# Kernel optimization log

Measured on AMD Instinct MI355X. Metric: run time of the kernel, lower is better.

Reference implementation:

```python
import jax, jax.numpy as jnp
import numpy as np

N_VAR, N_CONS = 100_000, 50_000
N_FEAS = N_VAR + N_CONS
E_OBJ, E_FEAS = 1_600_000, 2_400_000
H_OBJ = H_CONS = 64
C = H_OBJ + H_CONS  # concat_dim = 128
D = 256             # decoder_hidden_channels
NUM_GRAPHS = 64


def _gcn(x, src, dst, ew, W, b):
    # PyG GCNConv with edge weights: add self-loops (weight 1), sym-normalize, aggregate at dst.
    n = x.shape[0]
    loop = jnp.arange(n)
    src_f = jnp.concatenate([src, loop])
    dst_f = jnp.concatenate([dst, loop])
    ew_f = jnp.concatenate([ew, jnp.ones((n,), ew.dtype)])
    deg = jax.ops.segment_sum(ew_f, dst_f, num_segments=n)
    dinv = jnp.where(deg > 0, jax.lax.rsqrt(deg), 0.0)
    coef = dinv[src_f] * ew_f * dinv[dst_f]            # [E+n]
    h = x @ W                                          # [n, H]
    out = jax.ops.segment_sum(coef[:, None] * h[src_f], dst_f, num_segments=n)
    return out + b


def _mlp(z, W1, b1, W2, b2):
    return jnp.maximum(z @ W1 + b1, 0.0) @ W2 + b2


def setup_inputs() -> dict:
    key = jax.random.key(0)
    ks = iter(jax.random.split(key, 64))

    def nrm(shape, scale=1.0):
        return jax.random.normal(next(ks), shape, jnp.float32) * scale

    def lin(i, o):
        return nrm((i, o), 1.0 / np.sqrt(i)), jnp.zeros((o,), jnp.float32)

    inp = {}
    inp['x_obj'] = nrm((N_VAR, 4))
    inp['ei_obj'] = jax.random.randint(next(ks), (2, E_OBJ), 0, N_VAR)
    inp['ew_obj'] = jax.random.uniform(next(ks), (E_OBJ,), jnp.float32)
    inp['x_feas'] = nrm((N_FEAS, 4))
    inp['ei_feas'] = jax.random.randint(next(ks), (2, E_FEAS), 0, N_FEAS)
    inp['ew_feas'] = jax.random.uniform(next(ks), (E_FEAS,), jnp.float32)
    inp['batch_var'] = jnp.sort(jax.random.randint(next(ks), (N_VAR,), 0, NUM_GRAPHS))
    inp['n_var'] = N_VAR
    inp['n_bin'] = 50_000
    inp['c1o_W'], inp['c1o_b'] = lin(4, H_OBJ)
    inp['c2o_W'], inp['c2o_b'] = lin(H_OBJ, H_OBJ)
    inp['c1c_W'], inp['c1c_b'] = lin(4, H_CONS)
    inp['c2c_W'], inp['c2c_b'] = lin(H_CONS, H_CONS)
    inp['mu_W'], inp['mu_b'] = lin(C, C)
    inp['lv_W'], inp['lv_b'] = lin(C, C)
    inp['dx_W1'], inp['dx_b1'] = lin(C, D)
    inp['dx_W2'], inp['dx_b2'] = lin(D, 1)
    inp['dc_W1'], inp['dc_b1'] = lin(C, D)
    inp['dc_W2'], inp['dc_b2'] = lin(D, 1)
    inp['dk_W1'], inp['dk_b1'] = lin(C, D)
    inp['dk_W2'], inp['dk_b2'] = lin(D, 1)
    inp['di_W1'], inp['di_b1'] = lin(C, D)
    inp['di_W2'], inp['di_b2'] = lin(D, 1)
    return inp


def reference(x_obj, ei_obj, ew_obj, x_feas, ei_feas, ew_feas, batch_var, n_var, n_bin,
              c1o_W, c1o_b, c2o_W, c2o_b, c1c_W, c1c_b, c2c_W, c2c_b,
              mu_W, mu_b, lv_W, lv_b,
              dx_W1, dx_b1, dx_W2, dx_b2, dc_W1, dc_b1, dc_W2, dc_b2,
              dk_W1, dk_b1, dk_W2, dk_b2, di_W1, di_b1, di_W2, di_b2):
    so, do = ei_obj[0], ei_obj[1]
    sf, df = ei_feas[0], ei_feas[1]
    # objective encoder (all nodes are variables)
    h = jax.nn.relu(_gcn(x_obj, so, do, ew_obj, c1o_W, c1o_b))
    z_obj_var = jax.nn.relu(_gcn(h, so, do, ew_obj, c2o_W, c2o_b))
    # constraints encoder
    h = jax.nn.relu(_gcn(x_feas, sf, df, ew_feas, c1c_W, c1c_b))
    h = jax.nn.relu(_gcn(h, sf, df, ew_feas, c2c_W, c2c_b))
    z_cons_var = h[:n_var]          # variable_mask == first n_var nodes
    z_cons_constraints = h[n_var:]
    z_var = jnp.concatenate([z_obj_var, z_cons_var], axis=1)        # [N_var, C]
    z_cons_pad = jnp.pad(z_cons_constraints, ((0, 0), (0, C - z_cons_constraints.shape[1])))
    z_shared = jnp.concatenate([z_var, z_cons_pad], axis=0)         # [N_feas, C]
    z_mu = z_shared @ mu_W + mu_b
    z_logvar = z_shared @ lv_W + lv_b
    eps = jax.random.normal(jax.random.key(1), z_mu.shape, z_mu.dtype)
    z = z_mu + jnp.exp(0.5 * z_logvar) * eps
    z_var_s = z[:n_var]
    z_con_s = z[n_var:]
    x_hat = _mlp(z_var_s, dx_W1, dx_b1, dx_W2, dx_b2)[:, 0]
    # global_mean_pool over variable nodes
    sums = jax.ops.segment_sum(z_var_s, batch_var, num_segments=NUM_GRAPHS)
    cnts = jax.ops.segment_sum(jnp.ones((z_var_s.shape[0],), z.dtype), batch_var, num_segments=NUM_GRAPHS)
    pooled = sums / jnp.maximum(cnts, 1.0)[:, None]
    predicted_cost = _mlp(pooled, dc_W1, dc_b1, dc_W2, dc_b2)[:, 0]
    predicted_constraints = _mlp(z_con_s, dk_W1, dk_b1, dk_W2, dk_b2)[:, 0]
    integrality = jax.nn.sigmoid(_mlp(z_var_s, di_W1, di_b1, di_W2, di_b2))[:, 0]
    predicted_integrality = integrality[:n_bin]  # binary_mask == first n_bin variables
    return (x_hat, predicted_cost, predicted_constraints, predicted_integrality, z_mu, z_logvar)
```

## Files before the change

### kernel.cpp

```cpp
#include <hip/hip_runtime.h>
#include <math.h>

#define N_VAR_C  100000
#define N_CONS_C 50000
#define N_FEAS_C 150000
#define E_OBJ_C  1600000
#define E_FEAS_C 2400000
#define NG 64
#define N_BIN_C 50000
#define CAP 48

#define X_HAT_OFF 0
#define COST_OFF  100000
#define CONS_OFF  100064
#define INTG_OFF  150064
#define ZMU_OFF   200064
#define ZEL_TOTAL (N_FEAS_C * 128)
#define ZLV_OFF   (ZMU_OFF + ZEL_TOTAL)

static __device__ __forceinline__ unsigned rotl32(unsigned x, unsigned r) {
  return (x << r) | (x >> (32u - r));
}

static __device__ __forceinline__ void threefry01(unsigned x0, unsigned x1,
                                                  unsigned& o0, unsigned& o1) {
  const unsigned ks0 = 0u, ks1 = 1u, ks2 = 0x1BD11BDAu ^ 0u ^ 1u;
  x0 += ks0; x1 += ks1;
  x0 += x1; x1 = rotl32(x1, 13); x1 ^= x0;
  x0 += x1; x1 = rotl32(x1, 15); x1 ^= x0;
  x0 += x1; x1 = rotl32(x1, 26); x1 ^= x0;
  x0 += x1; x1 = rotl32(x1, 6);  x1 ^= x0;
  x0 += ks1; x1 += ks2 + 1u;
  x0 += x1; x1 = rotl32(x1, 17); x1 ^= x0;
  x0 += x1; x1 = rotl32(x1, 29); x1 ^= x0;
  x0 += x1; x1 = rotl32(x1, 16); x1 ^= x0;
  x0 += x1; x1 = rotl32(x1, 24); x1 ^= x0;
  x0 += ks2; x1 += ks0 + 2u;
  x0 += x1; x1 = rotl32(x1, 13); x1 ^= x0;
  x0 += x1; x1 = rotl32(x1, 15); x1 ^= x0;
  x0 += x1; x1 = rotl32(x1, 26); x1 ^= x0;
  x0 += x1; x1 = rotl32(x1, 6);  x1 ^= x0;
  x0 += ks0; x1 += ks1 + 3u;
  x0 += x1; x1 = rotl32(x1, 17); x1 ^= x0;
  x0 += x1; x1 = rotl32(x1, 29); x1 ^= x0;
  x0 += x1; x1 = rotl32(x1, 16); x1 ^= x0;
  x0 += x1; x1 = rotl32(x1, 24); x1 ^= x0;
  x0 += ks1; x1 += ks2 + 4u;
  x0 += x1; x1 = rotl32(x1, 13); x1 ^= x0;
  x0 += x1; x1 = rotl32(x1, 15); x1 ^= x0;
  x0 += x1; x1 = rotl32(x1, 26); x1 ^= x0;
  x0 += x1; x1 = rotl32(x1, 6);  x1 ^= x0;
  x0 += ks2; x1 += ks0 + 5u;
  o0 = x0; o1 = x1;
}

static __device__ __forceinline__ float bits_to_normal(unsigned b) {
  float f = __uint_as_float(0x3F800000u | (b >> 9)) - 1.0f;
  const float lo = -0.99999994f;
  float u = f * 2.0f + lo;
  u = fmaxf(lo, u);
  float w = -log1pf(-u * u);
  float p;
  if (w < 5.0f) {
    w -= 2.5f;
    p = 2.81022636e-08f;
    p = fmaf(p, w, 3.43273939e-07f);
    p = fmaf(p, w, -3.5233877e-06f);
    p = fmaf(p, w, -4.39150654e-06f);
    p = fmaf(p, w, 0.00021858087f);
    p = fmaf(p, w, -0.00125372503f);
    p = fmaf(p, w, -0.00417768164f);
    p = fmaf(p, w, 0.246640727f);
    p = fmaf(p, w, 1.50140941f);
  } else {
    w = sqrtf(w) - 3.0f;
    p = -0.000200214257f;
    p = fmaf(p, w, 0.000100950558f);
    p = fmaf(p, w, 0.00134934322f);
    p = fmaf(p, w, -0.00367342844f);
    p = fmaf(p, w, 0.00573950773f);
    p = fmaf(p, w, -0.0076224613f);
    p = fmaf(p, w, 0.00943887047f);
    p = fmaf(p, w, 1.00167406f);
    p = fmaf(p, w, 2.83297682f);
  }
  return 1.41421354f * (p * u);
}

__global__ __launch_bounds__(256) void fill_slots_kernel(
    const int* __restrict__ src, const int* __restrict__ dst,
    const float* __restrict__ ew, int* __restrict__ cnt,
    int2* __restrict__ slots, int E) {
  int e = blockIdx.x * 256 + threadIdx.x;
  if (e >= E) return;
  int d = dst[e];
  int p = atomicAdd(&cnt[d], 1);
  if (p < CAP) slots[(size_t)d * CAP + p] = make_int2(src[e], __float_as_int(ew[e]));
}

__global__ __launch_bounds__(256) void deg_kernel(
    const int2* __restrict__ slots, const int* __restrict__ cnt,
    float* __restrict__ dinv, int n) {
  int node = blockIdx.x * 4 + (threadIdx.x >> 6);
  if (node >= n) return;
  int lane = threadIdx.x & 63;
  int c = min(cnt[node], CAP);
  float v = 0.f;
  if (lane < c) v = __int_as_float(slots[(size_t)node * CAP + lane].y);
  for (int off = 32; off >= 1; off >>= 1) v += __shfl_down(v, off, 64);
  if (lane == 0) dinv[node] = 1.0f / sqrtf(v + 1.0f);
}

__global__ __launch_bounds__(256) void coef_kernel(
    int2* __restrict__ slots, const int* __restrict__ cnt,
    const float* __restrict__ dinv, int n) {
  int idx = blockIdx.x * 256 + threadIdx.x;
  if (idx >= n * CAP) return;
  int node = idx / CAP;
  int p = idx - node * CAP;
  if (p >= min(cnt[node], CAP)) return;
  int2 s = slots[idx];
  float coef = dinv[s.x] * __int_as_float(s.y) * dinv[node];
  slots[idx].y = __float_as_int(coef);
}

__global__ __launch_bounds__(256) void xw4_kernel(
    const float* __restrict__ x, const float* __restrict__ W,
    float* __restrict__ out, int n) {
  __shared__ float Ws[256];
  Ws[threadIdx.x] = W[threadIdx.x];
  __syncthreads();
  int gid = blockIdx.x * 256 + threadIdx.x;
  if (gid >= n * 64) return;
  int i = gid >> 6, c = gid & 63;
  float4 xv = *(const float4*)(x + i * 4);
  out[gid] = xv.x * Ws[c] + xv.y * Ws[64 + c] + xv.z * Ws[128 + c] + xv.w * Ws[192 + c];
}

__global__ __launch_bounds__(256) void gemm64_kernel(
    const float* __restrict__ h, const float* __restrict__ W,
    float* __restrict__ out, int n) {
  __shared__ float Ws[4096];
  __shared__ float hs[1024];
  for (int i = threadIdx.x; i < 4096; i += 256) Ws[i] = W[i];
  int r0 = blockIdx.x * 16;
  for (int i = threadIdx.x; i < 1024; i += 256) {
    int r = r0 + (i >> 6);
    hs[i] = (r < n) ? h[(size_t)r * 64 + (i & 63)] : 0.f;
  }
  __syncthreads();
  int tx = threadIdx.x & 63, ty = threadIdx.x >> 6;
  float a0 = 0, a1 = 0, a2 = 0, a3 = 0;
  for (int k = 0; k < 64; ++k) {
    float w = Ws[k * 64 + tx];
    a0 = fmaf(hs[ty * 64 + k], w, a0);
    a1 = fmaf(hs[(ty + 4) * 64 + k], w, a1);
    a2 = fmaf(hs[(ty + 8) * 64 + k], w, a2);
    a3 = fmaf(hs[(ty + 12) * 64 + k], w, a3);
  }
  int r = r0 + ty;
  if (r < n) out[(size_t)r * 64 + tx] = a0;
  r += 4; if (r < n) out[(size_t)r * 64 + tx] = a1;
  r += 4; if (r < n) out[(size_t)r * 64 + tx] = a2;
  r += 4; if (r < n) out[(size_t)r * 64 + tx] = a3;
}

__global__ __launch_bounds__(256) void agg_kernel(
    const float* __restrict__ t, const float* __restrict__ dinv,
    const int* __restrict__ cnt, const int2* __restrict__ slots,
    const float* __restrict__ bias, float* __restrict__ out, int n) {
  int node = blockIdx.x * 4 + (threadIdx.x >> 6);
  if (node >= n) return;
  int c = threadIdx.x & 63;
  float di = dinv[node];
  float acc = bias[c] + di * di * t[(size_t)node * 64 + c];
  const int2* sl = slots + (size_t)node * CAP;
  int pe = min(cnt[node], CAP);
  int p = 0;
  for (; p + 4 <= pe; p += 4) {
    int2 s0 = sl[p];
    int2 s1 = sl[p + 1];
    int2 s2 = sl[p + 2];
    int2 s3 = sl[p + 3];
    float t0 = t[(size_t)s0.x * 64 + c];
    float t1 = t[(size_t)s1.x * 64 + c];
    float t2 = t[(size_t)s2.x * 64 + c];
    float t3 = t[(size_t)s3.x * 64 + c];
    acc = fmaf(__int_as_float(s0.y), t0, acc);
    acc = fmaf(__int_as_float(s1.y), t1, acc);
    acc = fmaf(__int_as_float(s2.y), t2, acc);
    acc = fmaf(__int_as_float(s3.y), t3, acc);
  }
  for (; p < pe; ++p) {
    int2 s = sl[p];
    acc = fmaf(__int_as_float(s.y), t[(size_t)s.x * 64 + c], acc);
  }
  out[(size_t)node * 64 + c] = fmaxf(acc, 0.f);
}

__global__ __launch_bounds__(128) void mulv_kernel(
    const float* __restrict__ zobj, const float* __restrict__ hfeas,
    const float* __restrict__ muW, const float* __restrict__ mub,
    const float* __restrict__ lvW, const float* __restrict__ lvb,
    float* __restrict__ zmu, float* __restrict__ zlv) {
  int r0 = blockIdx.x * 8;
  int j = threadIdx.x;
  bool isvar = (r0 < N_VAR_C);
  float am[8], al[8];
  float mb = mub[j], lb = lvb[j];
#pragma unroll
  for (int r = 0; r < 8; ++r) { am[r] = mb; al[r] = lb; }
  const float* u0 = isvar ? zobj : hfeas;
  for (int k = 0; k < 64; ++k) {
    float wm = muW[k * 128 + j], wl = lvW[k * 128 + j];
#pragma unroll
    for (int r = 0; r < 8; ++r) {
      float zv = u0[(size_t)(r0 + r) * 64 + k];
      am[r] = fmaf(zv, wm, am[r]);
      al[r] = fmaf(zv, wl, al[r]);
    }
  }
  if (isvar) {
    for (int k = 0; k < 64; ++k) {
      float wm = muW[(64 + k) * 128 + j], wl = lvW[(64 + k) * 128 + j];
#pragma unroll
      for (int r = 0; r < 8; ++r) {
        float zv = hfeas[(size_t)(r0 + r) * 64 + k];
        am[r] = fmaf(zv, wm, am[r]);
        al[r] = fmaf(zv, wl, al[r]);
      }
    }
  }
#pragma unroll
  for (int r = 0; r < 8; ++r) {
    zmu[(size_t)(r0 + r) * 128 + j] = am[r];
    zlv[(size_t)(r0 + r) * 128 + j] = al[r];
  }
}

__global__ __launch_bounds__(256) void zgen_kernel(
    const float* __restrict__ zmu, const float* __restrict__ zlv, float* __restrict__ z) {
  int j = blockIdx.x * 256 + threadIdx.x;
  if (j >= ZEL_TOTAL) return;
  unsigned o0, o1;
  threefry01(0u, (unsigned)j, o0, o1);
  float e = bits_to_normal(o0 ^ o1);
  z[j] = fmaf(expf(0.5f * zlv[j]), e, zmu[j]);
}

#define POOL_ROWS 128
__global__ __launch_bounds__(256) void pool_accum_kernel(
    const float* __restrict__ z, const int* __restrict__ batch,
    float* __restrict__ sums, int* __restrict__ cnts) {
  int c = threadIdx.x & 127;
  int rsub = threadIdx.x >> 7;
  int r0 = blockIdx.x * POOL_ROWS;
  int rend = min(r0 + POOL_ROWS, N_VAR_C);
  float acc = 0.f;
  int cnt = 0;
  int cur = -1;
  for (int r = r0 + rsub; r < rend; r += 2) {
    int g = batch[r];
    if (g != cur) {
      if (cnt > 0) {
        atomicAdd(&sums[cur * 128 + c], acc);
        if (c == 0) atomicAdd(&cnts[cur], cnt);
      }
      acc = 0.f; cnt = 0; cur = g;
    }
    acc += z[(size_t)r * 128 + c];
    cnt++;
  }
  if (cnt > 0) {
    atomicAdd(&sums[cur * 128 + c], acc);
    if (c == 0) atomicAdd(&cnts[cur], cnt);
  }
}

__global__ __launch_bounds__(256) void pool_final_kernel(
    const float* __restrict__ sums, const int* __restrict__ cnts,
    float* __restrict__ pooled) {
  int i = blockIdx.x * 256 + threadIdx.x;
  if (i >= NG * 128) return;
  float cnt = (float)cnts[i >> 7];
  pooled[i] = sums[i] / fmaxf(cnt, 1.0f);
}

__global__ __launch_bounds__(128) void mlp_kernel(
    const float* __restrict__ in, const float* __restrict__ W1,
    const float* __restrict__ b1, const float* __restrict__ W2,
    const float* __restrict__ b2, float* __restrict__ out,
    int n, int rowoff, int sigmoid_out) {
  __shared__ float red[128];
  int r0 = blockIdx.x * 8;
  int j = threadIdx.x;
  float a0[8], a1[8];
  float b1a = b1[j], b1b = b1[j + 128];
#pragma unroll
  for (int r = 0; r < 8; ++r) { a0[r] = b1a; a1[r] = b1b; }
  const float* base = in + (size_t)(rowoff + r0) * 128;
  for (int k = 0; k < 128; ++k) {
    float w0 = W1[k * 256 + j], w1 = W1[k * 256 + 128 + j];
#pragma unroll
    for (int r = 0; r < 8; ++r) {
      float zv = base[r * 128 + k];
      a0[r] = fmaf(zv, w0, a0[r]);
      a1[r] = fmaf(zv, w1, a1[r]);
    }
  }
  float w2a = W2[j], w2b = W2[j + 128], bias2 = b2[0];
  for (int r = 0; r < 8; ++r) {
    float hv = fmaxf(a0[r], 0.f) * w2a + fmaxf(a1[r], 0.f) * w2b;
    red[j] = hv;
    __syncthreads();
    for (int off = 64; off >= 1; off >>= 1) {
      if (j < off) red[j] += red[j + off];
      __syncthreads();
    }
    if (j == 0 && (r0 + r) < n) {
      float o = red[0] + bias2;
      if (sigmoid_out) o = 1.0f / (1.0f + expf(-o));
      out[r0 + r] = o;
    }
    __syncthreads();
  }
}

extern "C" void kernel_launch(void* const* d_in, const int* in_sizes, int n_in,
                              void* d_out, int out_size, void* d_ws, size_t ws_size,
                              hipStream_t stream) {
  const float* x_obj   = (const float*)d_in[0];
  const int*   ei_obj  = (const int*)d_in[1];
  const float* ew_obj  = (const float*)d_in[2];
  const float* x_feas  = (const float*)d_in[3];
  const int*   ei_feas = (const int*)d_in[4];
  const float* ew_feas = (const float*)d_in[5];
  const int*   batch   = (const int*)d_in[6];
  const float* c1o_W = (const float*)d_in[9];
  const float* c1o_b = (const float*)d_in[10];
  const float* c2o_W = (const float*)d_in[11];
  const float* c2o_b = (const float*)d_in[12];
  const float* c1c_W = (const float*)d_in[13];
  const float* c1c_b = (const float*)d_in[14];
  const float* c2c_W = (const float*)d_in[15];
  const float* c2c_b = (const float*)d_in[16];
  const float* mu_W  = (const float*)d_in[17];
  const float* mu_b  = (const float*)d_in[18];
  const float* lv_W  = (const float*)d_in[19];
  const float* lv_b  = (const float*)d_in[20];
  const float* dx_W1 = (const float*)d_in[21];
  const float* dx_b1 = (const float*)d_in[22];
  const float* dx_W2 = (const float*)d_in[23];
  const float* dx_b2 = (const float*)d_in[24];
  const float* dc_W1 = (const float*)d_in[25];
  const float* dc_b1 = (const float*)d_in[26];
  const float* dc_W2 = (const float*)d_in[27];
  const float* dc_b2 = (const float*)d_in[28];
  const float* dk_W1 = (const float*)d_in[29];
  const float* dk_b1 = (const float*)d_in[30];
  const float* dk_W2 = (const float*)d_in[31];
  const float* dk_b2 = (const float*)d_in[32];
  const float* di_W1 = (const float*)d_in[33];
  const float* di_b1 = (const float*)d_in[34];
  const float* di_W2 = (const float*)d_in[35];
  const float* di_b2 = (const float*)d_in[36];

  float* out = (float*)d_out;
  char* ws = (char*)d_ws;
  size_t off = 0;
  auto alloc = [&](size_t bytes) -> char* {
    char* p = ws + off;
    off = (off + bytes + 255) & ~(size_t)255;
    return p;
  };

  float* Z = (float*)alloc(sizeof(float) * (size_t)N_FEAS_C * 128);
  float* A = Z;
  float* B = Z + (size_t)N_FEAS_C * 64;
  float* ZOBJ = (float*)alloc(sizeof(float) * (size_t)N_VAR_C * 64);
  int2* slots = (int2*)alloc(sizeof(int2) * (size_t)N_FEAS_C * CAP);
  float* dinv_o = (float*)alloc(sizeof(float) * N_VAR_C);
  float* dinv_f = (float*)alloc(sizeof(float) * N_FEAS_C);
  int* cnt_o = (int*)alloc(sizeof(int) * N_VAR_C);
  int* cnt_f = (int*)alloc(sizeof(int) * N_FEAS_C);
  float* psum   = (float*)alloc(sizeof(float) * NG * 128);
  int*   pcnt   = (int*)alloc(sizeof(int) * NG);
  float* pooled = (float*)alloc(sizeof(float) * NG * 128);

  float* zmu_out = out + ZMU_OFF;
  float* zlv_out = out + ZLV_OFF;

  const int* src_obj  = ei_obj;
  const int* dst_obj  = ei_obj + E_OBJ_C;
  const int* src_feas = ei_feas;
  const int* dst_feas = ei_feas + E_FEAS_C;

  hipMemsetAsync(cnt_o, 0, sizeof(int) * N_VAR_C, stream);
  hipMemsetAsync(cnt_f, 0, sizeof(int) * N_FEAS_C, stream);
  hipMemsetAsync(psum, 0, sizeof(float) * NG * 128, stream);
  hipMemsetAsync(pcnt, 0, sizeof(int) * NG, stream);

  fill_slots_kernel<<<(E_OBJ_C + 255) / 256, 256, 0, stream>>>(src_obj, dst_obj, ew_obj, cnt_o, slots, E_OBJ_C);
  deg_kernel<<<N_VAR_C / 4, 256, 0, stream>>>(slots, cnt_o, dinv_o, N_VAR_C);
  coef_kernel<<<(N_VAR_C * CAP + 255) / 256, 256, 0, stream>>>(slots, cnt_o, dinv_o, N_VAR_C);

  xw4_kernel<<<(N_VAR_C * 64 + 255) / 256, 256, 0, stream>>>(x_obj, c1o_W, A, N_VAR_C);
  agg_kernel<<<N_VAR_C / 4, 256, 0, stream>>>(A, dinv_o, cnt_o, slots, c1o_b, B, N_VAR_C);
  gemm64_kernel<<<N_VAR_C / 16, 256, 0, stream>>>(B, c2o_W, A, N_VAR_C);
  agg_kernel<<<N_VAR_C / 4, 256, 0, stream>>>(A, dinv_o, cnt_o, slots, c2o_b, ZOBJ, N_VAR_C);

  fill_slots_kernel<<<(E_FEAS_C + 255) / 256, 256, 0, stream>>>(src_feas, dst_feas, ew_feas, cnt_f, slots, E_FEAS_C);
  deg_kernel<<<N_FEAS_C / 4, 256, 0, stream>>>(slots, cnt_f, dinv_f, N_FEAS_C);
  coef_kernel<<<(N_FEAS_C * CAP + 255) / 256, 256, 0, stream>>>(slots, cnt_f, dinv_f, N_FEAS_C);

  xw4_kernel<<<(N_FEAS_C * 64 + 255) / 256, 256, 0, stream>>>(x_feas, c1c_W, A, N_FEAS_C);
  agg_kernel<<<N_FEAS_C / 4, 256, 0, stream>>>(A, dinv_f, cnt_f, slots, c1c_b, B, N_FEAS_C);
  gemm64_kernel<<<N_FEAS_C / 16, 256, 0, stream>>>(B, c2c_W, A, N_FEAS_C);
  agg_kernel<<<N_FEAS_C / 4, 256, 0, stream>>>(A, dinv_f, cnt_f, slots, c2c_b, B, N_FEAS_C);

  mulv_kernel<<<N_FEAS_C / 8, 128, 0, stream>>>(ZOBJ, B, mu_W, mu_b, lv_W, lv_b, zmu_out, zlv_out);

  zgen_kernel<<<(ZEL_TOTAL + 255) / 256, 256, 0, stream>>>(zmu_out, zlv_out, Z);

  pool_accum_kernel<<<(N_VAR_C + POOL_ROWS - 1) / POOL_ROWS, 256, 0, stream>>>(Z, batch, psum, pcnt);
  pool_final_kernel<<<(NG * 128 + 255) / 256, 256, 0, stream>>>(psum, pcnt, pooled);

  mlp_kernel<<<N_VAR_C / 8, 128, 0, stream>>>(Z, dx_W1, dx_b1, dx_W2, dx_b2, out + X_HAT_OFF, N_VAR_C, 0, 0);
  mlp_kernel<<<(NG + 7) / 8, 128, 0, stream>>>(pooled, dc_W1, dc_b1, dc_W2, dc_b2, out + COST_OFF, NG, 0, 0);
  mlp_kernel<<<N_CONS_C / 8, 128, 0, stream>>>(Z, dk_W1, dk_b1, dk_W2, dk_b2, out + CONS_OFF, N_CONS_C, N_VAR_C, 0);
  mlp_kernel<<<N_BIN_C / 8, 128, 0, stream>>>(Z, di_W1, di_b1, di_W2, di_b2, out + INTG_OFF, N_BIN_C, 0, 1);
}
```

Measured before the change: 1.467 ms.

## Store GCN pre-aggregation features in bf16 and double rows per block in GEMM kernels

```diff
diff --git a/kernel.cpp b/kernel.cpp
--- a/kernel.cpp
+++ b/kernel.cpp
@@ -17,6 +17,17 @@
 #define ZMU_OFF   200064
 #define ZEL_TOTAL (N_FEAS_C * 128)
 #define ZLV_OFF   (ZMU_OFF + ZEL_TOTAL)
+
+typedef unsigned short u16;
+
+static __device__ __forceinline__ float bf2f(u16 u) {
+  return __uint_as_float(((unsigned)u) << 16);
+}
+static __device__ __forceinline__ u16 f2bf(float f) {
+  unsigned x = __float_as_uint(f);
+  unsigned r = x + 0x7FFFu + ((x >> 16) & 1u);
+  return (u16)(r >> 16);
+}
 
 static __device__ __forceinline__ unsigned rotl32(unsigned x, unsigned r) {
   return (x << r) | (x >> (32u - r));
@@ -126,7 +137,7 @@
 
 __global__ __launch_bounds__(256) void xw4_kernel(
     const float* __restrict__ x, const float* __restrict__ W,
-    float* __restrict__ out, int n) {
+    u16* __restrict__ out, int n) {
   __shared__ float Ws[256];
   Ws[threadIdx.x] = W[threadIdx.x];
   __syncthreads();
@@ -134,12 +145,12 @@
   if (gid >= n * 64) return;
   int i = gid >> 6, c = gid & 63;
   float4 xv = *(const float4*)(x + i * 4);
-  out[gid] = xv.x * Ws[c] + xv.y * Ws[64 + c] + xv.z * Ws[128 + c] + xv.w * Ws[192 + c];
+  out[gid] = f2bf(xv.x * Ws[c] + xv.y * Ws[64 + c] + xv.z * Ws[128 + c] + xv.w * Ws[192 + c]);
 }
 
 __global__ __launch_bounds__(256) void gemm64_kernel(
     const float* __restrict__ h, const float* __restrict__ W,
-    float* __restrict__ out, int n) {
+    u16* __restrict__ out, int n) {
   __shared__ float Ws[4096];
   __shared__ float hs[1024];
   for (int i = threadIdx.x; i < 4096; i += 256) Ws[i] = W[i];
@@ -159,21 +170,21 @@
     a3 = fmaf(hs[(ty + 12) * 64 + k], w, a3);
   }
   int r = r0 + ty;
-  if (r < n) out[(size_t)r * 64 + tx] = a0;
-  r += 4; if (r < n) out[(size_t)r * 64 + tx] = a1;
-  r += 4; if (r < n) out[(size_t)r * 64 + tx] = a2;
-  r += 4; if (r < n) out[(size_t)r * 64 + tx] = a3;
+  if (r < n) out[(size_t)r * 64 + tx] = f2bf(a0);
+  r += 4; if (r < n) out[(size_t)r * 64 + tx] = f2bf(a1);
+  r += 4; if (r < n) out[(size_t)r * 64 + tx] = f2bf(a2);
+  r += 4; if (r < n) out[(size_t)r * 64 + tx] = f2bf(a3);
 }
 
 __global__ __launch_bounds__(256) void agg_kernel(
-    const float* __restrict__ t, const float* __restrict__ dinv,
+    const u16* __restrict__ t, const float* __restrict__ dinv,
     const int* __restrict__ cnt, const int2* __restrict__ slots,
     const float* __restrict__ bias, float* __restrict__ out, int n) {
   int node = blockIdx.x * 4 + (threadIdx.x >> 6);
   if (node >= n) return;
   int c = threadIdx.x & 63;
   float di = dinv[node];
-  float acc = bias[c] + di * di * t[(size_t)node * 64 + c];
+  float acc = bias[c] + di * di * bf2f(t[(size_t)node * 64 + c]);
   const int2* sl = slots + (size_t)node * CAP;
   int pe = min(cnt[node], CAP);
   int p = 0;
@@ -182,10 +193,10 @@
     int2 s1 = sl[p + 1];
     int2 s2 = sl[p + 2];
     int2 s3 = sl[p + 3];
-    float t0 = t[(size_t)s0.x * 64 + c];
-    float t1 = t[(size_t)s1.x * 64 + c];
-    float t2 = t[(size_t)s2.x * 64 + c];
-    float t3 = t[(size_t)s3.x * 64 + c];
+    float t0 = bf2f(t[(size_t)s0.x * 64 + c]);
+    float t1 = bf2f(t[(size_t)s1.x * 64 + c]);
+    float t2 = bf2f(t[(size_t)s2.x * 64 + c]);
+    float t3 = bf2f(t[(size_t)s3.x * 64 + c]);
     acc = fmaf(__int_as_float(s0.y), t0, acc);
     acc = fmaf(__int_as_float(s1.y), t1, acc);
     acc = fmaf(__int_as_float(s2.y), t2, acc);
@@ -193,7 +204,7 @@
   }
   for (; p < pe; ++p) {
     int2 s = sl[p];
-    acc = fmaf(__int_as_float(s.y), t[(size_t)s.x * 64 + c], acc);
+    acc = fmaf(__int_as_float(s.y), bf2f(t[(size_t)s.x * 64 + c]), acc);
   }
   out[(size_t)node * 64 + c] = fmaxf(acc, 0.f);
 }
@@ -203,18 +214,18 @@
     const float* __restrict__ muW, const float* __restrict__ mub,
     const float* __restrict__ lvW, const float* __restrict__ lvb,
     float* __restrict__ zmu, float* __restrict__ zlv) {
-  int r0 = blockIdx.x * 8;
+  int r0 = blockIdx.x * 16;
   int j = threadIdx.x;
   bool isvar = (r0 < N_VAR_C);
-  float am[8], al[8];
+  float am[16], al[16];
   float mb = mub[j], lb = lvb[j];
 #pragma unroll
-  for (int r = 0; r < 8; ++r) { am[r] = mb; al[r] = lb; }
+  for (int r = 0; r < 16; ++r) { am[r] = mb; al[r] = lb; }
   const float* u0 = isvar ? zobj : hfeas;
   for (int k = 0; k < 64; ++k) {
     float wm = muW[k * 128 + j], wl = lvW[k * 128 + j];
 #pragma unroll
-    for (int r = 0; r < 8; ++r) {
+    for (int r = 0; r < 16; ++r) {
       float zv = u0[(size_t)(r0 + r) * 64 + k];
       am[r] = fmaf(zv, wm, am[r]);
       al[r] = fmaf(zv, wl, al[r]);
@@ -224,7 +235,7 @@
     for (int k = 0; k < 64; ++k) {
       float wm = muW[(64 + k) * 128 + j], wl = lvW[(64 + k) * 128 + j];
 #pragma unroll
-      for (int r = 0; r < 8; ++r) {
+      for (int r = 0; r < 16; ++r) {
         float zv = hfeas[(size_t)(r0 + r) * 64 + k];
         am[r] = fmaf(zv, wm, am[r]);
         al[r] = fmaf(zv, wl, al[r]);
@@ -232,7 +243,7 @@
     }
   }
 #pragma unroll
-  for (int r = 0; r < 8; ++r) {
+  for (int r = 0; r < 16; ++r) {
     zmu[(size_t)(r0 + r) * 128 + j] = am[r];
     zlv[(size_t)(r0 + r) * 128 + j] = al[r];
   }
@@ -292,24 +303,24 @@
     const float* __restrict__ b2, float* __restrict__ out,
     int n, int rowoff, int sigmoid_out) {
   __shared__ float red[128];
-  int r0 = blockIdx.x * 8;
+  int r0 = blockIdx.x * 16;
   int j = threadIdx.x;
-  float a0[8], a1[8];
+  float a0[16], a1[16];
   float b1a = b1[j], b1b = b1[j + 128];
 #pragma unroll
-  for (int r = 0; r < 8; ++r) { a0[r] = b1a; a1[r] = b1b; }
+  for (int r = 0; r < 16; ++r) { a0[r] = b1a; a1[r] = b1b; }
   const float* base = in + (size_t)(rowoff + r0) * 128;
   for (int k = 0; k < 128; ++k) {
     float w0 = W1[k * 256 + j], w1 = W1[k * 256 + 128 + j];
 #pragma unroll
-    for (int r = 0; r < 8; ++r) {
+    for (int r = 0; r < 16; ++r) {
       float zv = base[r * 128 + k];
       a0[r] = fmaf(zv, w0, a0[r]);
       a1[r] = fmaf(zv, w1, a1[r]);
     }
   }
   float w2a = W2[j], w2b = W2[j + 128], bias2 = b2[0];
-  for (int r = 0; r < 8; ++r) {
+  for (int r = 0; r < 16; ++r) {
     float hv = fmaxf(a0[r], 0.f) * w2a + fmaxf(a1[r], 0.f) * w2b;
     red[j] = hv;
     __syncthreads();
@@ -375,9 +386,9 @@
   };
 
   float* Z = (float*)alloc(sizeof(float) * (size_t)N_FEAS_C * 128);
-  float* A = Z;
-  float* B = Z + (size_t)N_FEAS_C * 64;
-  float* ZOBJ = (float*)alloc(sizeof(float) * (size_t)N_VAR_C * 64);
+  float* B = Z;
+  float* ZOBJ = Z + (size_t)N_FEAS_C * 64;
+  u16* T = (u16*)alloc(sizeof(u16) * (size_t)N_FEAS_C * 64);
   int2* slots = (int2*)alloc(sizeof(int2) * (size_t)N_FEAS_C * CAP);
   float* dinv_o = (float*)alloc(sizeof(float) * N_VAR_C);
   float* dinv_f = (float*)alloc(sizeof(float) * N_FEAS_C);
@@ -404,29 +415,29 @@
   deg_kernel<<<N_VAR_C / 4, 256, 0, stream>>>(slots, cnt_o, dinv_o, N_VAR_C);
   coef_kernel<<<(N_VAR_C * CAP + 255) / 256, 256, 0, stream>>>(slots, cnt_o, dinv_o, N_VAR_C);
 
-  xw4_kernel<<<(N_VAR_C * 64 + 255) / 256, 256, 0, stream>>>(x_obj, c1o_W, A, N_VAR_C);
-  agg_kernel<<<N_VAR_C / 4, 256, 0, stream>>>(A, dinv_o, cnt_o, slots, c1o_b, B, N_VAR_C);
-  gemm64_kernel<<<N_VAR_C / 16, 256, 0, stream>>>(B, c2o_W, A, N_VAR_C);
-  agg_kernel<<<N_VAR_C / 4, 256, 0, stream>>>(A, dinv_o, cnt_o, slots, c2o_b, ZOBJ, N_VAR_C);
+  xw4_kernel<<<(N_VAR_C * 64 + 255) / 256, 256, 0, stream>>>(x_obj, c1o_W, T, N_VAR_C);
+  agg_kernel<<<N_VAR_C / 4, 256, 0, stream>>>(T, dinv_o, cnt_o, slots, c1o_b, B, N_VAR_C);
+  gemm64_kernel<<<N_VAR_C / 16, 256, 0, stream>>>(B, c2o_W, T, N_VAR_C);
+  agg_kernel<<<N_VAR_C / 4, 256, 0, stream>>>(T, dinv_o, cnt_o, slots, c2o_b, ZOBJ, N_VAR_C);
 
   fill_slots_kernel<<<(E_FEAS_C + 255) / 256, 256, 0, stream>>>(src_feas, dst_feas, ew_feas, cnt_f, slots, E_FEAS_C);
   deg_kernel<<<N_FEAS_C / 4, 256, 0, stream>>>(slots, cnt_f, dinv_f, N_FEAS_C);
   coef_kernel<<<(N_FEAS_C * CAP + 255) / 256, 256, 0, stream>>>(slots, cnt_f, dinv_f, N_FEAS_C);
 
-  xw4_kernel<<<(N_FEAS_C * 64 + 255) / 256, 256, 0, stream>>>(x_feas, c1c_W, A, N_FEAS_C);
-  agg_kernel<<<N_FEAS_C / 4, 256, 0, stream>>>(A, dinv_f, cnt_f, slots, c1c_b, B, N_FEAS_C);
-  gemm64_kernel<<<N_FEAS_C / 16, 256, 0, stream>>>(B, c2c_W, A, N_FEAS_C);
-  agg_kernel<<<N_FEAS_C / 4, 256, 0, stream>>>(A, dinv_f, cnt_f, slots, c2c_b, B, N_FEAS_C);
-
-  mulv_kernel<<<N_FEAS_C / 8, 128, 0, stream>>>(ZOBJ, B, mu_W, mu_b, lv_W, lv_b, zmu_out, zlv_out);
+  xw4_kernel<<<(N_FEAS_C * 64 + 255) / 256, 256, 0, stream>>>(x_feas, c1c_W, T, N_FEAS_C);
+  agg_kernel<<<N_FEAS_C / 4, 256, 0, stream>>>(T, dinv_f, cnt_f, slots, c1c_b, B, N_FEAS_C);
+  gemm64_kernel<<<N_FEAS_C / 16, 256, 0, stream>>>(B, c2c_W, T, N_FEAS_C);
+  agg_kernel<<<N_FEAS_C / 4, 256, 0, stream>>>(T, dinv_f, cnt_f, slots, c2c_b, B, N_FEAS_C);
+
+  mulv_kernel<<<N_FEAS_C / 16, 128, 0, stream>>>(ZOBJ, B, mu_W, mu_b, lv_W, lv_b, zmu_out, zlv_out);
 
   zgen_kernel<<<(ZEL_TOTAL + 255) / 256, 256, 0, stream>>>(zmu_out, zlv_out, Z);
 
   pool_accum_kernel<<<(N_VAR_C + POOL_ROWS - 1) / POOL_ROWS, 256, 0, stream>>>(Z, batch, psum, pcnt);
   pool_final_kernel<<<(NG * 128 + 255) / 256, 256, 0, stream>>>(psum, pcnt, pooled);
 
-  mlp_kernel<<<N_VAR_C / 8, 128, 0, stream>>>(Z, dx_W1, dx_b1, dx_W2, dx_b2, out + X_HAT_OFF, N_VAR_C, 0, 0);
-  mlp_kernel<<<(NG + 7) / 8, 128, 0, stream>>>(pooled, dc_W1, dc_b1, dc_W2, dc_b2, out + COST_OFF, NG, 0, 0);
-  mlp_kernel<<<N_CONS_C / 8, 128, 0, stream>>>(Z, dk_W1, dk_b1, dk_W2, dk_b2, out + CONS_OFF, N_CONS_C, N_VAR_C, 0);
-  mlp_kernel<<<N_BIN_C / 8, 128, 0, stream>>>(Z, di_W1, di_b1, di_W2, di_b2, out + INTG_OFF, N_BIN_C, 0, 1);
-}
+  mlp_kernel<<<N_VAR_C / 16, 128, 0, stream>>>(Z, dx_W1, dx_b1, dx_W2, dx_b2, out + X_HAT_OFF, N_VAR_C, 0, 0);
+  mlp_kernel<<<(NG + 15) / 16, 128, 0, stream>>>(pooled, dc_W1, dc_b1, dc_W2, dc_b2, out + COST_OFF, NG, 0, 0);
+  mlp_kernel<<<N_CONS_C / 16, 128, 0, stream>>>(Z, dk_W1, dk_b1, dk_W2, dk_b2, out + CONS_OFF, N_CONS_C, N_VAR_C, 0);
+  mlp_kernel<<<N_BIN_C / 16, 128, 0, stream>>>(Z, di_W1, di_b1, di_W2, di_b2, out + INTG_OFF, N_BIN_C, 0, 1);
+}
```

After: 1.954 ms. 33.2% more time.
